# Kernel tuning notes

Measured on AMD Instinct MI355X. Metric: run time of the kernel, lower is better.

## Reference

```python
import jax, jax.numpy as jnp
import numpy as np

B, H, W, N = 4, 64, 64, 64
NEAR, FAR = 2.0, 6.0
HID = 64


def setup_inputs() -> dict:
    key = jax.random.key(0)
    ks = jax.random.split(key, 6)
    ray_origins = jnp.tile(jnp.array([0.0, 0.0, 4.0], jnp.float32), (B, H, W, 1))
    ray_directions = jax.random.normal(ks[0], (B, H, W, 3), jnp.float32)
    tform_cam2world = jnp.eye(4, dtype=jnp.float32) + 0.1 * jax.random.normal(ks[1], (B, 4, 4), jnp.float32)
    depth_noise = jax.random.uniform(ks[2], (B, H, W, N), jnp.float32)
    u_samples = jax.random.uniform(ks[3], (B, H, W, N), jnp.float32)
    W1 = 0.5 * jax.random.normal(ks[4], (3, HID), jnp.float32)
    b1 = jnp.zeros((HID,), jnp.float32)
    W2 = 0.5 * jax.random.normal(ks[5], (HID, 4), jnp.float32)
    b2 = jnp.zeros((4,), jnp.float32)
    return dict(ray_origins=ray_origins, ray_directions=ray_directions,
                tform_cam2world=tform_cam2world, depth_noise=depth_noise,
                u_samples=u_samples, W1=W1, b1=b1, W2=W2, b2=b2)


def field(pts, W1, b1, W2, b2):
    # tiny radiance-field MLP standing in for the generator's sampler
    h = jax.nn.relu(pts @ W1 + b1)
    out = h @ W2 + b2
    sigma = out[..., 0]
    rgb = jax.nn.sigmoid(out[..., 1:4])
    return sigma, rgb


def compositing_weights(sigma, z_vals):
    # alpha-compositing weights (render_volume_density)
    dists = jnp.concatenate([z_vals[..., 1:] - z_vals[..., :-1],
                             jnp.full_like(z_vals[..., :1], 1e10)], axis=-1)
    alpha = 1.0 - jnp.exp(-jax.nn.relu(sigma) * dists)
    trans = jnp.cumprod(1.0 - alpha + 1e-10, axis=-1)
    trans = jnp.concatenate([jnp.ones_like(trans[..., :1]), trans[..., :-1]], axis=-1)
    return alpha * trans


def sample_pdf(bins, weights, u):
    # bins [R, M+1], weights [R, M], u [R, S] -> samples [R, S]
    pdf = weights / jnp.sum(weights, axis=-1, keepdims=True)
    cdf = jnp.cumsum(pdf, axis=-1)
    cdf = jnp.concatenate([jnp.zeros_like(cdf[..., :1]), cdf], axis=-1)  # [R, M+1]
    inds = jax.vmap(lambda c, uu: jnp.searchsorted(c, uu, side='right'))(cdf, u)
    last = cdf.shape[-1] - 1
    below = jnp.clip(inds - 1, 0, last)
    above = jnp.clip(inds, 0, last)
    cdf_b = jnp.take_along_axis(cdf, below, axis=-1)
    cdf_a = jnp.take_along_axis(cdf, above, axis=-1)
    bin_b = jnp.take_along_axis(bins, below, axis=-1)
    bin_a = jnp.take_along_axis(bins, above, axis=-1)
    denom = cdf_a - cdf_b
    denom = jnp.where(denom < 1e-5, 1.0, denom)
    t = (u - cdf_b) / denom
    return bin_b + t * (bin_a - bin_b)


def reference(ray_origins, ray_directions, tform_cam2world, depth_noise, u_samples, W1, b1, W2, b2):
    rd = ray_directions / jnp.linalg.norm(ray_directions, axis=-1, keepdims=True)
    # stratified coarse samples along each ray
    t = (jnp.arange(N, dtype=jnp.float32) + depth_noise) / N           # [B,H,W,N]
    z_vals = NEAR + (FAR - NEAR) * t
    pts = ray_origins[..., None, :] + rd[..., None, :] * z_vals[..., None]
    sigma, rgb = field(pts, W1, b1, W2, b2)                            # [B,H,W,N], [B,H,W,N,3]

    # --- hierarchical importance sampling (no_grad in original) ---
    w = compositing_weights(sigma, z_vals).reshape(-1, N)              # [R,N]
    pad = jnp.pad(w, ((0, 0), (1, 1)), constant_values=-jnp.inf)
    mx = jnp.maximum(pad[:, :-1], pad[:, 1:])                          # max_pool1d(k=2,s=1,p=1) -> [R,N+1]
    sm = 0.5 * (mx[:, :-1] + mx[:, 1:]) + 0.01                        # avg_pool1d(k=2,s=1)  -> [R,N]
    z_mid = (0.5 * (z_vals[..., 1:] + z_vals[..., :-1])).reshape(-1, N - 1)
    z_samples = sample_pdf(z_mid, sm[:, 1:-1], u_samples.reshape(-1, N))
    z_samples = jax.lax.stop_gradient(z_samples.reshape(B, H, W, N))

    # fine evaluation + merge-sort of coarse/fine samples
    z_all = jnp.concatenate([z_vals, z_samples], axis=-1)              # [B,H,W,2N]
    idx = jnp.argsort(z_all, axis=-1)
    z_sorted = jnp.take_along_axis(z_all, idx, axis=-1)
    pts_f = ray_origins[..., None, :] + rd[..., None, :] * z_samples[..., None]
    sigma_f, rgb_f = field(pts_f, W1, b1, W2, b2)
    sigma_all = jnp.take_along_axis(jnp.concatenate([sigma, sigma_f], axis=-1), idx, axis=-1)
    rgb_cat = jnp.concatenate([rgb, rgb_f], axis=-2)
    rgb_all = jnp.take_along_axis(rgb_cat, jnp.broadcast_to(idx[..., None], idx.shape + (3,)), axis=-2)

    # final alpha compositing
    w_all = compositing_weights(sigma_all, z_sorted)
    rgb_pred = jnp.sum(w_all[..., None] * rgb_all, axis=-2)            # [B,H,W,3]
    depth_pred = jnp.sum(w_all * z_sorted, axis=-1)                    # [B,H,W]
    mask_pred = jnp.sum(w_all, axis=-1)                                # [B,H,W]

    # camera-space depth (invert_space: R_w2c = R^T)
    R_w2c = jnp.swapaxes(tform_cam2world[:, :3, :3], -1, -2)           # [B,3,3]
    view_dir = jnp.einsum('bhwj,bij->bhwi', rd, R_w2c)
    depth_cam = -(view_dir * depth_pred[..., None])[..., -1]
    return rgb_pred, depth_cam, mask_pred
```

## Files before the change

kernel.cpp:

```cpp
#include <hip/hip_runtime.h>
#include <hip/hip_bf16.h>
#include <math.h>

#define Nn    64
#define RPB   4
#define NRAYS 16384
#define NEARV 2.0f
#define FARV  6.0f

typedef __attribute__((ext_vector_type(8))) short bf16x8;
typedef __attribute__((ext_vector_type(4))) float f32x4;
typedef __attribute__((ext_vector_type(2))) float f32x2;

template <int CTRL, int RMASK>
__device__ __forceinline__ float dpp_mv(float x, float ident) {
  return __int_as_float(__builtin_amdgcn_update_dpp(
      __float_as_int(ident), __float_as_int(x), CTRL, RMASK, 0xf, false));
}
__device__ __forceinline__ float shfl_up1(float x) {
  return __int_as_float(__builtin_amdgcn_update_dpp(
      __float_as_int(x), __float_as_int(x), 0x138, 0xf, 0xf, false));
}
__device__ __forceinline__ float shfl_dn1(float x) {
  return __int_as_float(__builtin_amdgcn_update_dpp(
      __float_as_int(x), __float_as_int(x), 0x130, 0xf, 0xf, false));
}
__device__ __forceinline__ float scan_add_dpp(float x) {
  x += dpp_mv<0x111, 0xf>(x, 0.f);
  x += dpp_mv<0x112, 0xf>(x, 0.f);
  x += dpp_mv<0x114, 0xf>(x, 0.f);
  x += dpp_mv<0x118, 0xf>(x, 0.f);
  x += dpp_mv<0x142, 0xa>(x, 0.f);
  x += dpp_mv<0x143, 0xc>(x, 0.f);
  return x;
}
__device__ __forceinline__ float scan_mul_dpp(float x) {
  x *= dpp_mv<0x111, 0xf>(x, 1.f);
  x *= dpp_mv<0x112, 0xf>(x, 1.f);
  x *= dpp_mv<0x114, 0xf>(x, 1.f);
  x *= dpp_mv<0x118, 0xf>(x, 1.f);
  x *= dpp_mv<0x142, 0xa>(x, 1.f);
  x *= dpp_mv<0x143, 0xc>(x, 1.f);
  return x;
}
__device__ __forceinline__ float reduce_add_bcast(float x) {
  x = scan_add_dpp(x);
  return __int_as_float(__builtin_amdgcn_readlane(__float_as_int(x), 63));
}

__device__ __forceinline__ float fast_rcp(float x) { return __builtin_amdgcn_rcpf(x); }
__device__ __forceinline__ float sigmoidf_fast(float x) { return fast_rcp(1.f + __expf(-x)); }

__device__ __forceinline__ short bfhi_bits(float x) { return (short)(__float_as_uint(x) >> 16); }
__device__ __forceinline__ float bfhi_val(float x)  { return __uint_as_float(__float_as_uint(x) & 0xFFFF0000u); }

template <int T>
__device__ __forceinline__ void rank_swz(unsigned kf, int& r) {
  const unsigned o = (unsigned)__builtin_amdgcn_ds_swizzle((int)kf, (T << 10) | 0x1F);
  r += (o < kf) ? 1 : 0;
  if constexpr (T + 1 < 32) rank_swz<T + 1>(kf, r);
}

__device__ __forceinline__ int count_lt_key(unsigned arr, unsigned x) {
  int cnt = 0;
#pragma unroll
  for (int step = 64; step >= 1; step >>= 1) {
    const int idx = cnt + step - 1;
    const unsigned v = (unsigned)__shfl((int)arr, idx, 64);
    if (idx < 64 && v < x) cnt += step;
  }
  return cnt;
}
__device__ __forceinline__ int count_le_f(float arr, float x) {
  int cnt = 0;
#pragma unroll
  for (int step = 64; step >= 1; step >>= 1) {
    const int idx = cnt + step - 1;
    const float v = __shfl(arr, idx, 64);
    if (idx < 63 && v <= x) cnt += step;
  }
  return cnt;
}

__device__ __forceinline__ void field_eval(
    float zlane, const f32x2 c0v[2][4], const f32x2 c1v[2][4],
    const bf16x8 aHi[2], const bf16x8 aLo[2],
    float b20, float b21, float b22, float b23,
    int quad, int col, float4* scratch, float o[4]) {
#pragma unroll
  for (int nt = 0; nt < 4; ++nt) {
    f32x4 acc = {0.f, 0.f, 0.f, 0.f};
    const float zm = __shfl(zlane, nt * 16 + col, 64);
    const f32x2 zm2 = {zm, zm};
#pragma unroll
    for (int ks = 0; ks < 2; ++ks) {
      union { bf16x8 v; unsigned u[4]; } Bhi, Blo;
#pragma unroll
      for (int p = 0; p < 4; ++p) {
        f32x2 h = zm2 * c1v[ks][p] + c0v[ks][p];
        h = __builtin_elementwise_max(h, (f32x2){0.f, 0.f});
        union { f32x2 f; unsigned u[2]; } U; U.f = h;
        Bhi.u[p] = __builtin_amdgcn_perm(U.u[1], U.u[0], 0x07060302u);
        union { unsigned u[2]; f32x2 f; } M;
        M.u[0] = U.u[0] & 0xFFFF0000u;
        M.u[1] = U.u[1] & 0xFFFF0000u;
        const f32x2 l = h - M.f;
        union { f32x2 f; unsigned u[2]; } L; L.f = l;
        Blo.u[p] = __builtin_amdgcn_perm(L.u[1], L.u[0], 0x07060302u);
      }
      acc = __builtin_amdgcn_mfma_f32_16x16x32_bf16(aHi[ks], Bhi.v, acc, 0, 0, 0);
      acc = __builtin_amdgcn_mfma_f32_16x16x32_bf16(aHi[ks], Blo.v, acc, 0, 0, 0);
      acc = __builtin_amdgcn_mfma_f32_16x16x32_bf16(aLo[ks], Bhi.v, acc, 0, 0, 0);
    }
    if (quad == 0) scratch[nt * 16 + col] = make_float4(acc[0], acc[1], acc[2], acc[3]);
  }
  const float4 r = scratch[(threadIdx.x & 63)];
  o[0] = r.x + b20; o[1] = r.y + b21; o[2] = r.z + b22; o[3] = r.w + b23;
}

__global__ __launch_bounds__(RPB * 64, 4) void nerf_fused(
    const float* __restrict__ ray_o, const float* __restrict__ ray_d,
    const float* __restrict__ tform, const float* __restrict__ noise,
    const float* __restrict__ usmp,  const float* __restrict__ W1,
    const float* __restrict__ b1,    const float* __restrict__ W2,
    const float* __restrict__ b2,    float* __restrict__ out) {
  const int wave = threadIdx.x >> 6;
  const int lane = threadIdx.x & 63;
  const int ray  = blockIdx.x * RPB + wave;
  const int quad = lane >> 4;
  const int col  = lane & 15;

  __shared__ float2 sC [RPB][Nn];
  __shared__ float  sZs[RPB][2 * Nn];
  __shared__ float4 sPk[RPB][2 * Nn];

  const float o0 = ray_o[ray * 3 + 0], o1 = ray_o[ray * 3 + 1], o2 = ray_o[ray * 3 + 2];
  float d0 = ray_d[ray * 3 + 0], d1 = ray_d[ray * 3 + 1], d2 = ray_d[ray * 3 + 2];
  const float rn = __builtin_amdgcn_rsqf(d0 * d0 + d1 * d1 + d2 * d2);
  d0 *= rn; d1 *= rn; d2 *= rn;

  {
    const float w10 = W1[lane], w11 = W1[64 + lane], w12 = W1[128 + lane];
    const float c1 = d0 * w10 + d1 * w11 + d2 * w12;
    const float c0 = o0 * w10 + o1 * w11 + o2 * w12 + b1[lane];
    sC[wave][lane] = make_float2(c0, c1);
  }

  const float nz = noise[ray * Nn + lane];
  const float z  = NEARV + (FARV - NEARV) * ((float)lane + nz) * (1.0f / Nn);
  const unsigned kc = ((__float_as_uint(z) - 0x40000000u) << 7) | (unsigned)lane;

  f32x2 c0v[2][4], c1v[2][4];
#pragma unroll
  for (int ks = 0; ks < 2; ++ks) {
    const float4* cc4 = (const float4*)&sC[wave][0];
    const int base4 = (ks * 32 + quad * 8) >> 1;
#pragma unroll
    for (int jj = 0; jj < 4; ++jj) {
      const float4 v = cc4[base4 + jj];
      c0v[ks][jj] = (f32x2){v.x, v.z};
      c1v[ks][jj] = (f32x2){v.y, v.w};
    }
  }

  bf16x8 aHi[2], aLo[2];
#pragma unroll
  for (int ks = 0; ks < 2; ++ks) {
#pragma unroll
    for (int j = 0; j < 8; ++j) {
      const int k = ks * 32 + quad * 8 + j;
      const float wv  = (col < 4) ? W2[k * 4 + col] : 0.f;
      aHi[ks][j] = bfhi_bits(wv);
      aLo[ks][j] = bfhi_bits(wv - bfhi_val(wv));
    }
  }
  const float b20 = b2[0], b21 = b2[1], b22 = b2[2], b23 = b2[3];
  float4* scratch = &sPk[wave][0];

  float oc[4];
  field_eval(z, c0v, c1v, aHi, aLo, b20, b21, b22, b23, quad, col, scratch, oc);
  const float sig = oc[0];
  const float cr = sigmoidf_fast(oc[1]), cg = sigmoidf_fast(oc[2]), cb = sigmoidf_fast(oc[3]);

  const float zn   = shfl_dn1(z);
  const float dist = (lane == 63) ? 1e10f : (zn - z);
  const float alpha = 1.f - __expf(-fmaxf(sig, 0.f) * dist);
  float cdfreg, binreg;
  {
    const float P  = scan_mul_dpp(1.f - alpha + 1e-10f);
    float Te = shfl_up1(P);
    if (lane == 0) Te = 1.f;
    const float w = alpha * Te;

    const float mxA = fmaxf(shfl_up1(w), w);
    const float mxB = fmaxf(w, shfl_dn1(w));
    const float sm = 0.5f * (mxA + mxB) + 0.01f;

    const float v   = (lane >= 1 && lane <= 62) ? sm : 0.f;
    const float tot = reduce_add_bcast(v);
    const float pdf = v * fast_rcp(tot);
    const float C   = scan_add_dpp(pdf);
    cdfreg = (lane == 0) ? 0.f : C;
    binreg = 0.5f * (z + zn);
  }

  const float u = usmp[ray * Nn + lane];
  const int lo = count_le_f(cdfreg, u);
  const int below = lo - 1;
  const int above = (lo < 63) ? lo : 62;
  const float cdfb = __shfl(cdfreg, below, 64);
  const float cdfa = __shfl(cdfreg, above, 64);
  const float binb = __shfl(binreg, below, 64);
  const float bina = __shfl(binreg, above, 64);
  float den = cdfa - cdfb;
  if (den < 1e-5f) den = 1.f;
  const float zs = fmaf((u - cdfb) * fast_rcp(den), bina - binb, binb);

  float of[4];
  field_eval(zs, c0v, c1v, aHi, aLo, b20, b21, b22, b23, quad, col, scratch, of);
  const float sigF = of[0];
  const float fr = sigmoidf_fast(of[1]), fg = sigmoidf_fast(of[2]), fb = sigmoidf_fast(of[3]);

  const unsigned kf = ((__float_as_uint(zs) - 0x40000000u) << 7) | (unsigned)(64 + lane);

  int r1 = 0;
  rank_swz<1>(kf, r1);
  const int xaddr = (lane ^ 32) << 2;
#pragma unroll
  for (int s = 0; s < 32; ++s) {
    const unsigned o = (unsigned)__builtin_amdgcn_ds_bpermute(xaddr ^ (s << 2), (int)kf);
    r1 += (o < kf) ? 1 : 0;
  }

  const int lo1 = count_lt_key(kc, kf);
  const unsigned kfS = (unsigned)__builtin_amdgcn_ds_permute(r1 << 2, (int)kf);
  const int lo2 = count_lt_key(kfS, kc);
  const int p0 = lane + lo2;
  const int p1 = r1 + lo1;

  sZs[wave][p0] = z;
  sZs[wave][p1] = zs;
  sPk[wave][p0] = make_float4(sig,  cr, cg, cb);
  sPk[wave][p1] = make_float4(sigF, fr, fg, fb);

  const float2 zz = *(const float2*)&sZs[wave][2 * lane];
  const float z0 = zz.x, z1 = zz.y;
  const float z2 = shfl_dn1(z0);
  const float dist0 = z1 - z0;
  const float dist1 = (lane == 63) ? 1e10f : (z2 - z1);
  const float4 q0 = sPk[wave][2 * lane];
  const float4 q1 = sPk[wave][2 * lane + 1];
  const float al0 = 1.f - __expf(-fmaxf(q0.x, 0.f) * dist0);
  const float al1 = 1.f - __expf(-fmaxf(q1.x, 0.f) * dist1);
  const float aa0 = 1.f - al0 + 1e-10f;
  const float aa1 = 1.f - al1 + 1e-10f;
  const float Pp = scan_mul_dpp(aa0 * aa1);
  float Tp = shfl_up1(Pp);
  if (lane == 0) Tp = 1.f;
  const float w0 = al0 * Tp;
  const float w1 = al1 * Tp * aa0;

  const float accR = reduce_add_bcast(w0 * q0.y + w1 * q1.y);
  const float accG = reduce_add_bcast(w0 * q0.z + w1 * q1.z);
  const float accB = reduce_add_bcast(w0 * q0.w + w1 * q1.w);
  const float accD = reduce_add_bcast(w0 * z0 + w1 * z1);
  const float accM = reduce_add_bcast(w0 + w1);

  if (lane == 0) {
    const float* tf = tform + (ray >> 12) * 16;
    const float vz = d0 * tf[2] + d1 * tf[6] + d2 * tf[10];
    out[ray * 3 + 0]     = accR;
    out[ray * 3 + 1]     = accG;
    out[ray * 3 + 2]     = accB;
    out[NRAYS * 3 + ray] = -vz * accD;
    out[NRAYS * 4 + ray] = accM;
  }
}

extern "C" void kernel_launch(void* const* d_in, const int* in_sizes, int n_in,
                              void* d_out, int out_size, void* d_ws, size_t ws_size,
                              hipStream_t stream) {
  const float* ray_o = (const float*)d_in[0];
  const float* ray_d = (const float*)d_in[1];
  const float* tform = (const float*)d_in[2];
  const float* noise = (const float*)d_in[3];
  const float* usmp  = (const float*)d_in[4];
  const float* W1    = (const float*)d_in[5];
  const float* b1    = (const float*)d_in[6];
  const float* W2    = (const float*)d_in[7];
  const float* b2    = (const float*)d_in[8];
  float* out = (float*)d_out;

  nerf_fused<<<dim3(NRAYS / RPB), RPB * 64, 0, stream>>>(
      ray_o, ray_d, tform, noise, usmp, W1, b1, W2, b2, out);
}
```

Measured before the change: 109.4 us.

## Replace rank-counting sort with bitonic network and drop split-B MFMA for fine samples

The O(64) all-pairs rank computation for the fine-sample keys is replaced with a 21-stage bitonic sorting network using swizzle and bpermute, and each lane's rank is recovered by an inverse permute. The second field evaluation now rounds the hidden activations to a single bf16 value instead of splitting them into hi and lo parts, which removes one of three MFMAs per k-step and the split arithmetic. The aim is to cut cross-lane traffic and matrix-core work. In exchange the fine-sample MLP output loses precision, which could push results past tolerance.

```diff
diff --git a/kernel.cpp b/kernel.cpp
--- a/kernel.cpp
+++ b/kernel.cpp
@@ -54,12 +54,28 @@
 __device__ __forceinline__ short bfhi_bits(float x) { return (short)(__float_as_uint(x) >> 16); }
 __device__ __forceinline__ float bfhi_val(float x)  { return __uint_as_float(__float_as_uint(x) & 0xFFFF0000u); }
 
-template <int T>
-__device__ __forceinline__ void rank_swz(unsigned kf, int& r) {
-  const unsigned o = (unsigned)__builtin_amdgcn_ds_swizzle((int)kf, (T << 10) | 0x1F);
-  r += (o < kf) ? 1 : 0;
-  if constexpr (T + 1 < 32) rank_swz<T + 1>(kf, r);
-}
+template <int LEVEL, int D>
+__device__ __forceinline__ void bitonic_stage(unsigned& k, int lane) {
+  unsigned t;
+  if constexpr (D == 32) {
+    t = (unsigned)__builtin_amdgcn_ds_bpermute((lane ^ 32) << 2, (int)k);
+  } else {
+    t = (unsigned)__builtin_amdgcn_ds_swizzle((int)k, (D << 10) | 0x1F);
+  }
+  const bool bitd = (lane & D) != 0;
+  const bool desc = (lane & (1 << LEVEL)) != 0;
+  const unsigned mn = (k < t) ? k : t;
+  const unsigned mx = (k < t) ? t : k;
+  k = (bitd == desc) ? mn : mx;
+}
+template <int LEVEL, int D>
+struct BSort {
+  static __device__ __forceinline__ void run(unsigned& k, int lane) {
+    bitonic_stage<LEVEL, D>(k, lane);
+    if constexpr (D > 1) BSort<LEVEL, D / 2>::run(k, lane);
+    else if constexpr (LEVEL < 6) BSort<LEVEL + 1, (1 << LEVEL)>::run(k, lane);
+  }
+};
 
 __device__ __forceinline__ int count_lt_key(unsigned arr, unsigned x) {
   int cnt = 0;
@@ -82,6 +98,7 @@
   return cnt;
 }
 
+template <bool SPLITB>
 __device__ __forceinline__ void field_eval(
     float zlane, const f32x2 c0v[2][4], const f32x2 c1v[2][4],
     const bf16x8 aHi[2], const bf16x8 aLo[2],
@@ -99,18 +116,28 @@
       for (int p = 0; p < 4; ++p) {
         f32x2 h = zm2 * c1v[ks][p] + c0v[ks][p];
         h = __builtin_elementwise_max(h, (f32x2){0.f, 0.f});
-        union { f32x2 f; unsigned u[2]; } U; U.f = h;
-        Bhi.u[p] = __builtin_amdgcn_perm(U.u[1], U.u[0], 0x07060302u);
-        union { unsigned u[2]; f32x2 f; } M;
-        M.u[0] = U.u[0] & 0xFFFF0000u;
-        M.u[1] = U.u[1] & 0xFFFF0000u;
-        const f32x2 l = h - M.f;
-        union { f32x2 f; unsigned u[2]; } L; L.f = l;
-        Blo.u[p] = __builtin_amdgcn_perm(L.u[1], L.u[0], 0x07060302u);
+        if constexpr (SPLITB) {
+          union { f32x2 f; unsigned u[2]; } U; U.f = h;
+          Bhi.u[p] = __builtin_amdgcn_perm(U.u[1], U.u[0], 0x07060302u);
+          union { unsigned u[2]; f32x2 f; } M;
+          M.u[0] = U.u[0] & 0xFFFF0000u;
+          M.u[1] = U.u[1] & 0xFFFF0000u;
+          const f32x2 l = h - M.f;
+          union { f32x2 f; unsigned u[2]; } L; L.f = l;
+          Blo.u[p] = __builtin_amdgcn_perm(L.u[1], L.u[0], 0x07060302u);
+        } else {
+          __hip_bfloat162 t = __float22bfloat162_rn(make_float2(h[0], h[1]));
+          Bhi.u[p] = *reinterpret_cast<unsigned*>(&t);
+        }
       }
-      acc = __builtin_amdgcn_mfma_f32_16x16x32_bf16(aHi[ks], Bhi.v, acc, 0, 0, 0);
-      acc = __builtin_amdgcn_mfma_f32_16x16x32_bf16(aHi[ks], Blo.v, acc, 0, 0, 0);
-      acc = __builtin_amdgcn_mfma_f32_16x16x32_bf16(aLo[ks], Bhi.v, acc, 0, 0, 0);
+      if constexpr (SPLITB) {
+        acc = __builtin_amdgcn_mfma_f32_16x16x32_bf16(aHi[ks], Bhi.v, acc, 0, 0, 0);
+        acc = __builtin_amdgcn_mfma_f32_16x16x32_bf16(aHi[ks], Blo.v, acc, 0, 0, 0);
+        acc = __builtin_amdgcn_mfma_f32_16x16x32_bf16(aLo[ks], Bhi.v, acc, 0, 0, 0);
+      } else {
+        acc = __builtin_amdgcn_mfma_f32_16x16x32_bf16(aHi[ks], Bhi.v, acc, 0, 0, 0);
+        acc = __builtin_amdgcn_mfma_f32_16x16x32_bf16(aLo[ks], Bhi.v, acc, 0, 0, 0);
+      }
     }
     if (quad == 0) scratch[nt * 16 + col] = make_float4(acc[0], acc[1], acc[2], acc[3]);
   }
@@ -178,7 +205,7 @@
   float4* scratch = &sPk[wave][0];
 
   float oc[4];
-  field_eval(z, c0v, c1v, aHi, aLo, b20, b21, b22, b23, quad, col, scratch, oc);
+  field_eval<true>(z, c0v, c1v, aHi, aLo, b20, b21, b22, b23, quad, col, scratch, oc);
   const float sig = oc[0];
   const float cr = sigmoidf_fast(oc[1]), cg = sigmoidf_fast(oc[2]), cb = sigmoidf_fast(oc[3]);
 
@@ -217,23 +244,17 @@
   const float zs = fmaf((u - cdfb) * fast_rcp(den), bina - binb, binb);
 
   float of[4];
-  field_eval(zs, c0v, c1v, aHi, aLo, b20, b21, b22, b23, quad, col, scratch, of);
+  field_eval<false>(zs, c0v, c1v, aHi, aLo, b20, b21, b22, b23, quad, col, scratch, of);
   const float sigF = of[0];
   const float fr = sigmoidf_fast(of[1]), fg = sigmoidf_fast(of[2]), fb = sigmoidf_fast(of[3]);
 
   const unsigned kf = ((__float_as_uint(zs) - 0x40000000u) << 7) | (unsigned)(64 + lane);
 
-  int r1 = 0;
-  rank_swz<1>(kf, r1);
-  const int xaddr = (lane ^ 32) << 2;
-#pragma unroll
-  for (int s = 0; s < 32; ++s) {
-    const unsigned o = (unsigned)__builtin_amdgcn_ds_bpermute(xaddr ^ (s << 2), (int)kf);
-    r1 += (o < kf) ? 1 : 0;
-  }
+  unsigned kfS = kf;
+  BSort<1, 1>::run(kfS, lane);
+  const int r1 = __builtin_amdgcn_ds_permute((int)((kfS & 63u) << 2), lane);
 
   const int lo1 = count_lt_key(kc, kf);
-  const unsigned kfS = (unsigned)__builtin_amdgcn_ds_permute(r1 << 2, (int)kf);
   const int lo2 = count_lt_key(kfS, kc);
   const int p0 = lane + lo2;
   const int p1 = r1 + lo1;
```

After: 104.4 us. 4.6% less time.
